# Kernel optimization log

Measured on AMD Instinct MI355X. Metric: run time of the kernel, lower is better.

The kernel has to match this reference:

```python
import jax, jax.numpy as jnp
import numpy as np

# Standard SMPL kinematic tree parents (kintree_table)
PARENTS = np.array([-1, 0, 0, 0, 1, 2, 3, 4, 5, 6, 7, 8, 9, 9, 9,
                    12, 13, 14, 16, 17, 18, 19, 20, 21])
NV, NJ, NB, NP = 6890, 24, 10, 207


def rodrigues(r):
    """Axis-angle [N,3] -> rotation matrices [N,3,3] (Rodrigues formula)."""
    theta = jnp.linalg.norm(r, axis=1, keepdims=True) + 1e-8  # [N,1]
    rh = r / theta                                            # [N,3]
    cos = jnp.cos(theta)[..., None]                           # [N,1,1]
    sin = jnp.sin(theta)[..., None]
    z = jnp.zeros_like(rh[:, 0])
    m = jnp.stack([z, -rh[:, 2], rh[:, 1],
                   rh[:, 2], z, -rh[:, 0],
                   -rh[:, 1], rh[:, 0], z], axis=1).reshape(-1, 3, 3)
    dot = rh[:, :, None] * rh[:, None, :]                     # outer product
    eye = jnp.eye(3, dtype=r.dtype)
    return cos * eye + (1.0 - cos) * dot + sin * m


def setup_inputs() -> dict:
    key = jax.random.key(0)
    ks = jax.random.split(key, 9)
    B = 512
    betas = jax.random.normal(ks[0], (B, NB), dtype=jnp.float32)
    thetas = jax.random.normal(ks[1], (B, NJ * 3), dtype=jnp.float32) * 0.3
    trans = jax.random.normal(ks[2], (B, 3), dtype=jnp.float32)
    scale = jnp.ones((1,), dtype=jnp.float32)
    v_template = jax.random.normal(ks[3], (NV, 3), dtype=jnp.float32)
    shapedirs = jax.random.normal(ks[4], (NV, 3, NB), dtype=jnp.float32) * 0.01
    posedirs = jax.random.normal(ks[5], (NV, 3, NP), dtype=jnp.float32) * 0.01
    Jr = jax.random.uniform(ks[6], (NJ, NV), dtype=jnp.float32)
    J_regressor = Jr / jnp.sum(Jr, axis=1, keepdims=True)
    w = jax.random.uniform(ks[7], (NV, NJ), dtype=jnp.float32)
    weights = w / jnp.sum(w, axis=1, keepdims=True)
    return {"betas": betas, "thetas": thetas, "trans": trans, "scale": scale,
            "v_template": v_template, "shapedirs": shapedirs,
            "posedirs": posedirs, "J_regressor": J_regressor,
            "weights": weights}


def reference(betas, thetas, trans, scale, v_template, shapedirs, posedirs,
              J_regressor, weights):
    B = betas.shape[0]
    dt = betas.dtype
    # Shape blend shapes: v_shaped [B, 6890, 3]
    v_shaped = jnp.einsum('bs,vcs->bvc', betas, shapedirs) + v_template
    # Rest-pose joints J(beta): [B, 24, 3]
    J = jnp.einsum('jv,bvc->bjc', J_regressor, v_shaped)
    # Local rotations from axis-angle, root scaled by `scale`
    lRs = rodrigues(thetas.reshape(-1, 3)).reshape(B, NJ, 3, 3)
    lRs = lRs.at[:, 0].multiply(scale[0])
    # Local joint offsets: root keeps J[:,0], children use J[i] - J[parent[i]]
    parents = jnp.asarray(PARENTS)
    t = J - J[:, jnp.clip(parents, 0)]
    t = t.at[:, 0].set(J[:, 0])
    # Local 4x4 transforms [B, 24, 4, 4]
    top = jnp.concatenate([lRs, t[..., None]], axis=3)          # [B,24,3,4]
    bottom = jnp.broadcast_to(jnp.array([0., 0., 0., 1.], dtype=dt),
                              (B, NJ, 1, 4))
    A = jnp.concatenate([top, bottom], axis=2)
    # Kinematic chain accumulation (fixed 24-joint tree)
    results = [A[:, 0]]
    for i in range(1, NJ):
        results.append(results[PARENTS[i]] @ A[:, i])
    stacked = jnp.stack(results, axis=1)                         # [B,24,4,4]
    # Remove rest-pose joint locations from translation column
    Jh = jnp.concatenate([J, jnp.zeros((B, NJ, 1), dtype=dt)], axis=2)
    deformed = jnp.einsum('bjxy,bjy->bjx', stacked, Jh)          # [B,24,4]
    G = stacked.at[..., 3].add(-deformed)
    # Pose blend shapes from non-root rotations
    lrotmin = (lRs[:, 1:] - jnp.eye(3, dtype=dt)).reshape(B, -1)  # [B,207]
    v_posed = v_shaped + jnp.einsum('bp,vcp->bvc', lrotmin, posedirs)
    # Linear blend skinning
    T = jnp.einsum('bjxy,vj->bvxy', G, weights)                  # [B,6890,4,4]
    vh = jnp.concatenate([v_posed, jnp.ones((B, NV, 1), dtype=dt)], axis=2)
    v = jnp.einsum('bvxy,bvy->bvx', T, vh)[:, :, :3]
    result = v + trans[:, None, :]
    joints = jnp.einsum('jv,bvc->bjc', J_regressor, result)
    return result, joints
```

## Files before the change

kernel.cpp:

```cpp
#include <hip/hip_runtime.h>

#define NVERT 6890
#define NJNT  24
#define NBETA 10
#define NPOSE 207
#define NBATCH 512
#define KPAD 224
#define MROWS 20736
#define NVC (NVERT * 3)

#define NBA 18144
#define NBW 1728
#define NJR 576

typedef __attribute__((ext_vector_type(8))) short short8;
typedef __attribute__((ext_vector_type(4))) float floatx4;

__constant__ int c_par[NJNT]   = {-1,0,0,0,1,2,3,4,5,6,7,8,9,9,9,12,13,14,16,17,18,19,20,21};
__constant__ int c_depth[NJNT] = { 0,1,1,1,2,2,2,3,3,3,4,4,4,4,4,5,5,5,6,6,7,7,8,8};

static __device__ __forceinline__ unsigned short f2bf(float x) {
  union { float f; unsigned u; } v; v.f = x;
  unsigned r = (v.u + 0x7FFFu + ((v.u >> 16) & 1u)) >> 16;
  return (unsigned short)r;
}
static __device__ __forceinline__ float bf2f(unsigned short h) {
  union { unsigned u; float f; } v; v.u = (unsigned)h << 16;
  return v.f;
}

typedef __attribute__((address_space(1))) const void as1_void;
typedef __attribute__((address_space(3))) void as3_void;
static __device__ __forceinline__ void gl_lds16(const void* g, void* l) {
  __builtin_amdgcn_global_load_lds((as1_void*)g, (as3_void*)l, 16, 0, 0);
}

__global__ __launch_bounds__(256) void k_prep(
    const float* __restrict__ pdir, const float* __restrict__ sd,
    const float* __restrict__ vt, const float* __restrict__ wgt,
    const float* __restrict__ Jr,
    unsigned short* __restrict__ AT, unsigned short* __restrict__ W16,
    float* __restrict__ wsJP) {
  const int bx = blockIdx.x;
  const int tid = threadIdx.x;
  if (bx < NBA) {
    const int idx = bx * 256 + tid;
    const int kk = idx & 31;
    const int row = (idx >> 5) % MROWS;
    const int kt = idx / (MROWS * 32);
    const int k = kt * 32 + kk;
    float val = 0.f;
    if (row < NVC) {
      if (k < NPOSE)            val = pdir[(size_t)row * NPOSE + k];
      else if (k < NPOSE + 10)  val = sd[(size_t)row * 10 + (k - NPOSE)];
      else if (k == NPOSE + 10) val = vt[row];
    }
    AT[idx] = f2bf(val);
  } else if (bx < NBA + NBW) {
    const int idx = (bx - NBA) * 256 + tid;
    const int v = idx >> 6, c = idx & 63, j = c & 31;
    const float w = (v < NVERT && j < 24) ? wgt[(size_t)v * 24 + j] : 0.f;
    const unsigned short hi = f2bf(w);
    W16[idx] = (c >> 5) ? f2bf(w - bf2f(hi)) : hi;
  } else {
    const int jb = bx - (NBA + NBW);
    const int jc = jb % 72, j = jc / 3, c = jc % 3;
    const int chunk = jb / 72;
    const int v0 = chunk * 864;
    const int vend = min(NVERT, v0 + 864);
    float acc[11];
    #pragma unroll
    for (int k = 0; k < 11; ++k) acc[k] = 0.f;
    for (int v = v0 + tid; v < vend; v += 256) {
      const float w = Jr[j * NVERT + v];
      acc[0] += w * vt[v * 3 + c];
      const float* s = sd + (size_t)v * 30 + c * 10;
      #pragma unroll
      for (int k = 0; k < 10; ++k) acc[1 + k] += w * s[k];
    }
    #pragma unroll
    for (int off = 32; off > 0; off >>= 1) {
      #pragma unroll
      for (int k = 0; k < 11; ++k) acc[k] += __shfl_down(acc[k], off, 64);
    }
    __shared__ float red[4][11];
    const int lane = tid & 63, wv = tid >> 6;
    if (lane == 0) {
      #pragma unroll
      for (int k = 0; k < 11; ++k) red[wv][k] = acc[k];
    }
    __syncthreads();
    if (tid == 0) {
      #pragma unroll
      for (int k = 0; k < 11; ++k)
        wsJP[(size_t)(chunk * 72 + jc) * 11 + k] =
            red[0][k] + red[1][k] + red[2][k] + red[3][k];
    }
  }
}

__global__ __launch_bounds__(256, 2) void k_chain3(
    const float* __restrict__ betas, const float* __restrict__ thetas,
    const float* __restrict__ scale, const float* __restrict__ trans,
    const float* __restrict__ wsJP,
    unsigned short* __restrict__ BT, unsigned short* __restrict__ G16) {
  __shared__ __align__(16) float sJ[792];
  __shared__ __align__(16) float sJJ[4][72];
  __shared__ __align__(16) float sM[4][288];
  __shared__ __align__(16) unsigned short sG[4][1024];
  __shared__ __align__(16) unsigned short sB[4][KPAD];

  const int tid = threadIdx.x;
  const int wv = tid >> 6, lane = tid & 63;
  const int b = blockIdx.x * 4 + wv;

  if (tid < 72) {
    #pragma unroll
    for (int k = 0; k < 11; ++k) {
      float s = 0.f;
      #pragma unroll
      for (int c8 = 0; c8 < 8; ++c8) s += wsJP[(size_t)(c8 * 72 + tid) * 11 + k];
      if (k == 0) sJ[tid] = s;
      else        sJ[72 + tid * 10 + (k - 1)] = s;
    }
  }
  #pragma unroll
  for (int r = 0; r < 4; ++r) {
    sG[wv][lane * 16 + r * 4 + 0] = 0; sG[wv][lane * 16 + r * 4 + 1] = 0;
    sG[wv][lane * 16 + r * 4 + 2] = 0; sG[wv][lane * 16 + r * 4 + 3] = 0;
  }
  __syncthreads();

  float R[9], t[3], M[12], Jx = 0.f, Jy = 0.f, Jz = 0.f;
  const int i = lane;
  if (i < NJNT) {
    #pragma unroll
    for (int c = 0; c < 3; ++c) {
      float a = sJ[i * 3 + c];
      const float* d = sJ + 72 + (i * 3 + c) * 10;
      #pragma unroll
      for (int s = 0; s < NBETA; ++s) a += d[s] * betas[b * NBETA + s];
      if (c == 0) Jx = a; else if (c == 1) Jy = a; else Jz = a;
    }
    sJJ[wv][i * 3 + 0] = Jx; sJJ[wv][i * 3 + 1] = Jy; sJJ[wv][i * 3 + 2] = Jz;
    const float rx = thetas[b * 72 + i * 3 + 0];
    const float ry = thetas[b * 72 + i * 3 + 1];
    const float rz = thetas[b * 72 + i * 3 + 2];
    const float th = sqrtf(rx * rx + ry * ry + rz * rz) + 1e-8f;
    const float inv = 1.f / th;
    const float x = rx * inv, y = ry * inv, z = rz * inv;
    const float cs = cosf(th), sn = sinf(th), omc = 1.f - cs;
    R[0] = cs + omc * x * x;     R[1] = omc * x * y - sn * z; R[2] = omc * x * z + sn * y;
    R[3] = omc * x * y + sn * z; R[4] = cs + omc * y * y;     R[5] = omc * y * z - sn * x;
    R[6] = omc * x * z - sn * y; R[7] = omc * y * z + sn * x; R[8] = cs + omc * z * z;
    if (i == 0) {
      const float sc = scale[0];
      #pragma unroll
      for (int k = 0; k < 9; ++k) R[k] *= sc;
    } else {
      #pragma unroll
      for (int k = 0; k < 9; ++k)
        sB[wv][(i - 1) * 9 + k] = f2bf(R[k] - ((k == 0 || k == 4 || k == 8) ? 1.f : 0.f));
    }
  }
  if (i == 0) {
    #pragma unroll
    for (int s = 0; s < NBETA; ++s) sB[wv][NPOSE + s] = f2bf(betas[b * NBETA + s]);
    sB[wv][NPOSE + 10] = 0x3F80;
    #pragma unroll
    for (int k = NPOSE + 11; k < KPAD; ++k) sB[wv][k] = 0;
  }
  __syncthreads();

  if (i < NJNT) {
    if (i == 0) { t[0] = Jx; t[1] = Jy; t[2] = Jz; }
    else {
      const int p = c_par[i];
      t[0] = Jx - sJJ[wv][p * 3 + 0];
      t[1] = Jy - sJJ[wv][p * 3 + 1];
      t[2] = Jz - sJJ[wv][p * 3 + 2];
    }
    if (i == 0) {
      #pragma unroll
      for (int r = 0; r < 3; ++r) {
        M[r*4+0] = R[r*3+0]; M[r*4+1] = R[r*3+1]; M[r*4+2] = R[r*3+2]; M[r*4+3] = t[r];
      }
      #pragma unroll
      for (int k = 0; k < 12; ++k) sM[wv][k] = M[k];
    }
  }
  __syncthreads();

  for (int lvl = 1; lvl <= 8; ++lvl) {
    if (i < NJNT && c_depth[i] == lvl) {
      const float* Mp = sM[wv] + c_par[i] * 12;
      #pragma unroll
      for (int r = 0; r < 3; ++r) {
        const float p0 = Mp[r*4+0], p1 = Mp[r*4+1], p2 = Mp[r*4+2], p3 = Mp[r*4+3];
        M[r*4+0] = p0*R[0] + p1*R[3] + p2*R[6];
        M[r*4+1] = p0*R[1] + p1*R[4] + p2*R[7];
        M[r*4+2] = p0*R[2] + p1*R[5] + p2*R[8];
        M[r*4+3] = p0*t[0] + p1*t[1] + p2*t[2] + p3;
      }
      #pragma unroll
      for (int k = 0; k < 12; ++k) sM[wv][i * 12 + k] = M[k];
    }
    __syncthreads();
  }

  if (i < NJNT) {
    #pragma unroll
    for (int r = 0; r < 3; ++r) {
      M[r*4+3] = M[r*4+3] - (M[r*4+0]*Jx + M[r*4+1]*Jy + M[r*4+2]*Jz)
               + trans[b * 3 + r];
    }
    #pragma unroll
    for (int e = 0; e < 12; ++e) {
      const float g = M[e];
      const unsigned short hi = f2bf(g);
      sG[wv][e * 32 + i]       = hi;
      sG[wv][512 + e * 32 + i] = f2bf(g - bf2f(hi));
    }
  }
  __syncthreads();

  *(uint4*)(G16 + (size_t)b * 1024 + lane * 16)     = *(uint4*)&sG[wv][lane * 16];
  *(uint4*)(G16 + (size_t)b * 1024 + lane * 16 + 8) = *(uint4*)&sG[wv][lane * 16 + 8];
  if (lane < 28)
    *(uint4*)(BT + ((size_t)(lane >> 2) * NBATCH + b) * 32 + (lane & 3) * 8) =
        *(uint4*)&sB[wv][lane * 8];
}

__global__ __launch_bounds__(256, 3) void k_skin4(
    const unsigned short* __restrict__ AT, const unsigned short* __restrict__ BT,
    const unsigned short* __restrict__ W16, const unsigned short* __restrict__ G16,
    float* __restrict__ out) {
  __shared__ __align__(16) char smem[33536];
  float* sV           = (float*)smem;
  unsigned short* sG2 = (unsigned short*)(smem + 13056);

  const int tid = threadIdx.x;
  const int wv = tid >> 6, lane = tid & 63;
  const int q = lane >> 4, n = lane & 15;

  const int fb = blockIdx.x;
  const int vb = (fb & 7) * 108 + (fb >> 3);
  const int b0 = (vb & 7) * 64;
  const int by = vb >> 3;
  const int vc0 = by * 192;

  floatx4 acc[3][4];
  #pragma unroll
  for (int mt = 0; mt < 3; ++mt)
    #pragma unroll
    for (int nt = 0; nt < 4; ++nt) acc[mt][nt] = (floatx4)(0.f);

  const int stoff = (lane >> 2) * 32 + (((lane & 3) ^ ((lane >> 3) & 3)) * 8);
  const int rslot = ((lane >> 4) ^ ((lane >> 1) & 3)) * 8;

  const unsigned short* gA0 = AT + ((size_t)vc0 + 48 * wv) * 32 + stoff;
  const unsigned short* gB0 = BT + ((size_t)b0 + 16 * wv) * 32 + stoff;

  {
    unsigned short* la = (unsigned short*)smem + 48 * wv * 32;
    unsigned short* lb = (unsigned short*)(smem + 12288) + 16 * wv * 32;
    gl_lds16(gA0,        la);
    gl_lds16(gA0 + 512,  la + 512);
    gl_lds16(gA0 + 1024, la + 1024);
    gl_lds16(gB0,        lb);
  }
  __syncthreads();

  int cur = 0;
  for (int kt = 0; kt < 7; ++kt) {
    if (kt < 6) {
      const int nb = (cur ^ 1) << 14;
      unsigned short* la = (unsigned short*)(smem + nb) + 48 * wv * 32;
      unsigned short* lb = (unsigned short*)(smem + nb + 12288) + 16 * wv * 32;
      const unsigned short* ga = gA0 + (size_t)(kt + 1) * MROWS * 32;
      const unsigned short* gb = gB0 + (size_t)(kt + 1) * NBATCH * 32;
      gl_lds16(ga,        la);
      gl_lds16(ga + 512,  la + 512);
      gl_lds16(ga + 1024, la + 1024);
      gl_lds16(gb,        lb);
    }
    const unsigned short* sAc = (const unsigned short*)(smem + (cur << 14));
    const unsigned short* sBc = sAc + 6144;
    short8 af[3], bfr[4];
    #pragma unroll
    for (int mt = 0; mt < 3; ++mt)
      af[mt] = *(const short8*)(sAc + (48 * wv + 16 * mt + n) * 32 + rslot);
    #pragma unroll
    for (int nt = 0; nt < 4; ++nt)
      bfr[nt] = *(const short8*)(sBc + (16 * nt + n) * 32 + rslot);
    #pragma unroll
    for (int mt = 0; mt < 3; ++mt)
      #pragma unroll
      for (int nt = 0; nt < 4; ++nt)
        acc[mt][nt] = __builtin_amdgcn_mfma_f32_16x16x32_bf16(
            af[mt], bfr[nt], acc[mt][nt], 0, 0, 0);
    __syncthreads();
    cur ^= 1;
  }

  short8 wh[4], wl[4];
  #pragma unroll
  for (int vt = 0; vt < 4; ++vt) {
    const unsigned short* wr = W16 + (size_t)(by * 64 + vt * 16 + n) * 64;
    wh[vt] = *(const short8*)(wr + q * 8);
    wl[vt] = *(const short8*)(wr + 32 + q * 8);
  }

  for (int nt = 0; nt < 4; ++nt) {
    for (int s = 0; s < 2; ++s) {
      __syncthreads();
      if (s == 0) {
        #pragma unroll
        for (int mt = 0; mt < 3; ++mt)
          #pragma unroll
          for (int r = 0; r < 4; ++r)
            sV[(48 * wv + 16 * mt + 4 * q + r) * 17 + n] = acc[mt][nt][r];
      }
      const int bg0 = b0 + nt * 16 + s * 8;
      for (int i = tid; i < 1024; i += 256) {
        const int row = i >> 2, c4 = i & 3;
        const int t = row >> 5, rem = row & 31;
        *(uint4*)(sG2 + row * 40 + c4 * 8) =
            *(const uint4*)(G16 + (size_t)(bg0 + t) * 1024 + rem * 32 + c4 * 8);
      }
      __syncthreads();
      #pragma unroll
      for (int bb = 0; bb < 2; ++bb) {
        const int t = wv * 2 + bb;
        const int col = s * 8 + t;
        const int bg = b0 + nt * 16 + col;
        const short8 gh = *(const short8*)(sG2 + (t * 32 + n) * 40 + q * 8);
        const short8 gl = *(const short8*)(sG2 + (t * 32 + 16 + n) * 40 + q * 8);
        #pragma unroll
        for (int vt = 0; vt < 4; ++vt) {
          floatx4 a2 = (floatx4)(0.f);
          a2 = __builtin_amdgcn_mfma_f32_16x16x32_bf16(gh, wl[vt], a2, 0, 0, 0);
          a2 = __builtin_amdgcn_mfma_f32_16x16x32_bf16(gl, wh[vt], a2, 0, 0, 0);
          a2 = __builtin_amdgcn_mfma_f32_16x16x32_bf16(gh, wh[vt], a2, 0, 0, 0);
          const float X = sV[(48 * vt + 3 * n + 0) * 17 + col];
          const float Y = sV[(48 * vt + 3 * n + 1) * 17 + col];
          const float Z = sV[(48 * vt + 3 * n + 2) * 17 + col];
          const float o = a2[0] * X + a2[1] * Y + a2[2] * Z + a2[3];
          const int vc = vc0 + 48 * vt + 3 * n + q;
          if (q < 3 && vc < NVC)
            out[(size_t)bg * NVC + vc] = o;
        }
      }
    }
  }
}

__global__ __launch_bounds__(256) void k_jnt1(
    const float* __restrict__ Jr, const float* __restrict__ res,
    float* __restrict__ wsJ2) {
  const int b0 = blockIdx.x * 2;
  const int chunk = blockIdx.y;
  const int v0 = chunk * 864;
  const int vend = min(NVERT, v0 + 864);
  const int lane = threadIdx.x & 63, wv = threadIdx.x >> 6;
  float acc[36];
  #pragma unroll
  for (int k = 0; k < 36; ++k) acc[k] = 0.f;
  const float* rA = res + (size_t)b0 * NVC;
  const float* rB = res + (size_t)(b0 + 1) * NVC;
  for (int v = v0 + lane; v < vend; v += 64) {
    const float a0 = rA[v * 3 + 0], a1 = rA[v * 3 + 1], a2 = rA[v * 3 + 2];
    const float e0 = rB[v * 3 + 0], e1 = rB[v * 3 + 1], e2 = rB[v * 3 + 2];
    #pragma unroll
    for (int k = 0; k < 6; ++k) {
      const int j = wv + 4 * k;
      const float w = Jr[j * NVERT + v];
      acc[k*6+0] += w * a0; acc[k*6+1] += w * a1; acc[k*6+2] += w * a2;
      acc[k*6+3] += w * e0; acc[k*6+4] += w * e1; acc[k*6+5] += w * e2;
    }
  }
  #pragma unroll
  for (int off = 32; off > 0; off >>= 1) {
    #pragma unroll
    for (int k = 0; k < 36; ++k) acc[k] += __shfl_down(acc[k], off, 64);
  }
  if (lane == 0) {
    #pragma unroll
    for (int k = 0; k < 6; ++k) {
      const int j = wv + 4 * k;
      float* d0 = wsJ2 + ((size_t)b0 * 8 + chunk) * 72 + j * 3;
      d0[0] = acc[k*6+0]; d0[1] = acc[k*6+1]; d0[2] = acc[k*6+2];
      float* d1 = wsJ2 + ((size_t)(b0 + 1) * 8 + chunk) * 72 + j * 3;
      d1[0] = acc[k*6+3]; d1[1] = acc[k*6+4]; d1[2] = acc[k*6+5];
    }
  }
}

__global__ __launch_bounds__(256) void k_jnt2(
    const float* __restrict__ wsJ2, float* __restrict__ joints) {
  const int idx = blockIdx.x * 256 + threadIdx.x;
  const int b = idx / 72, jc = idx - b * 72;
  float s = 0.f;
  #pragma unroll
  for (int c8 = 0; c8 < 8; ++c8)
    s += wsJ2[((size_t)b * 8 + c8) * 72 + jc];
  joints[idx] = s;
}

extern "C" void kernel_launch(void* const* d_in, const int* in_sizes, int n_in,
                              void* d_out, int out_size, void* d_ws, size_t ws_size,
                              hipStream_t stream) {
  const float* betas  = (const float*)d_in[0];
  const float* thetas = (const float*)d_in[1];
  const float* trans  = (const float*)d_in[2];
  const float* scale  = (const float*)d_in[3];
  const float* vtpl   = (const float*)d_in[4];
  const float* sd     = (const float*)d_in[5];
  const float* pdir   = (const float*)d_in[6];
  const float* Jr     = (const float*)d_in[7];
  const float* wgt    = (const float*)d_in[8];
  float* out = (float*)d_out;

  float* ws   = (float*)d_ws;
  float* wsJP = ws;
  unsigned short* AT  = (unsigned short*)(ws + 6336);
  unsigned short* BT  = AT + (size_t)MROWS * KPAD;
  unsigned short* W16 = BT + (size_t)NBATCH * KPAD;
  unsigned short* G16 = W16 + (size_t)6912 * 64;
  float* wsJ2 = (float*)AT;

  k_prep<<<NBA + NBW + NJR, 256, 0, stream>>>(pdir, sd, vtpl, wgt, Jr, AT, W16, wsJP);
  k_chain3<<<NBATCH / 4, 256, 0, stream>>>(betas, thetas, scale, trans, wsJP, BT, G16);
  k_skin4<<<864, 256, 0, stream>>>(AT, BT, W16, G16, out);
  k_jnt1<<<dim3(NBATCH / 2, 8), 256, 0, stream>>>(Jr, out, wsJ2);
  k_jnt2<<<(NBATCH * 72) / 256, 256, 0, stream>>>(wsJ2, out + (size_t)NBATCH * NVC);
}
```

Baseline: 173.9 us.

## Halve skinning batch tile and replace joint reduction kernel with atomics

```diff
diff --git a/kernel.cpp b/kernel.cpp
--- a/kernel.cpp
+++ b/kernel.cpp
@@ -103,7 +103,8 @@
     const float* __restrict__ betas, const float* __restrict__ thetas,
     const float* __restrict__ scale, const float* __restrict__ trans,
     const float* __restrict__ wsJP,
-    unsigned short* __restrict__ BT, unsigned short* __restrict__ G16) {
+    unsigned short* __restrict__ BT, unsigned short* __restrict__ G16,
+    float* __restrict__ jzero) {
   __shared__ __align__(16) float sJ[792];
   __shared__ __align__(16) float sJJ[4][72];
   __shared__ __align__(16) float sM[4][288];
@@ -113,6 +114,9 @@
   const int tid = threadIdx.x;
   const int wv = tid >> 6, lane = tid & 63;
   const int b = blockIdx.x * 4 + wv;
+
+  for (int z = blockIdx.x * 256 + tid; z < NBATCH * 72; z += 32768)
+    jzero[z] = 0.f;
 
   if (tid < 72) {
     #pragma unroll
@@ -231,7 +235,7 @@
         *(uint4*)&sB[wv][lane * 8];
 }
 
-__global__ __launch_bounds__(256, 3) void k_skin4(
+__global__ __launch_bounds__(256, 4) void k_skin4(
     const unsigned short* __restrict__ AT, const unsigned short* __restrict__ BT,
     const unsigned short* __restrict__ W16, const unsigned short* __restrict__ G16,
     float* __restrict__ out) {
@@ -244,16 +248,16 @@
   const int q = lane >> 4, n = lane & 15;
 
   const int fb = blockIdx.x;
-  const int vb = (fb & 7) * 108 + (fb >> 3);
-  const int b0 = (vb & 7) * 64;
-  const int by = vb >> 3;
+  const int vb = (fb & 7) * 216 + (fb >> 3);
+  const int b0 = (vb & 15) * 32;
+  const int by = vb >> 4;
   const int vc0 = by * 192;
 
-  floatx4 acc[3][4];
+  floatx4 acc[3][2];
   #pragma unroll
   for (int mt = 0; mt < 3; ++mt)
     #pragma unroll
-    for (int nt = 0; nt < 4; ++nt) acc[mt][nt] = (floatx4)(0.f);
+    for (int nt = 0; nt < 2; ++nt) acc[mt][nt] = (floatx4)(0.f);
 
   const int stoff = (lane >> 2) * 32 + (((lane & 3) ^ ((lane >> 3) & 3)) * 8);
   const int rslot = ((lane >> 4) ^ ((lane >> 1) & 3)) * 8;
@@ -263,40 +267,43 @@
 
   {
     unsigned short* la = (unsigned short*)smem + 48 * wv * 32;
-    unsigned short* lb = (unsigned short*)(smem + 12288) + 16 * wv * 32;
     gl_lds16(gA0,        la);
     gl_lds16(gA0 + 512,  la + 512);
     gl_lds16(gA0 + 1024, la + 1024);
-    gl_lds16(gB0,        lb);
+    if (wv < 2) {
+      unsigned short* lb = (unsigned short*)(smem + 12288) + 16 * wv * 32;
+      gl_lds16(gB0, lb);
+    }
   }
   __syncthreads();
 
   int cur = 0;
   for (int kt = 0; kt < 7; ++kt) {
     if (kt < 6) {
-      const int nb = (cur ^ 1) << 14;
+      const int nb = (cur ^ 1) * 14336;
       unsigned short* la = (unsigned short*)(smem + nb) + 48 * wv * 32;
-      unsigned short* lb = (unsigned short*)(smem + nb + 12288) + 16 * wv * 32;
       const unsigned short* ga = gA0 + (size_t)(kt + 1) * MROWS * 32;
-      const unsigned short* gb = gB0 + (size_t)(kt + 1) * NBATCH * 32;
       gl_lds16(ga,        la);
       gl_lds16(ga + 512,  la + 512);
       gl_lds16(ga + 1024, la + 1024);
-      gl_lds16(gb,        lb);
-    }
-    const unsigned short* sAc = (const unsigned short*)(smem + (cur << 14));
+      if (wv < 2) {
+        unsigned short* lb = (unsigned short*)(smem + nb + 12288) + 16 * wv * 32;
+        gl_lds16(gB0 + (size_t)(kt + 1) * NBATCH * 32, lb);
+      }
+    }
+    const unsigned short* sAc = (const unsigned short*)(smem + cur * 14336);
     const unsigned short* sBc = sAc + 6144;
-    short8 af[3], bfr[4];
+    short8 af[3], bfr[2];
     #pragma unroll
     for (int mt = 0; mt < 3; ++mt)
       af[mt] = *(const short8*)(sAc + (48 * wv + 16 * mt + n) * 32 + rslot);
     #pragma unroll
-    for (int nt = 0; nt < 4; ++nt)
+    for (int nt = 0; nt < 2; ++nt)
       bfr[nt] = *(const short8*)(sBc + (16 * nt + n) * 32 + rslot);
     #pragma unroll
     for (int mt = 0; mt < 3; ++mt)
       #pragma unroll
-      for (int nt = 0; nt < 4; ++nt)
+      for (int nt = 0; nt < 2; ++nt)
         acc[mt][nt] = __builtin_amdgcn_mfma_f32_16x16x32_bf16(
             af[mt], bfr[nt], acc[mt][nt], 0, 0, 0);
     __syncthreads();
@@ -311,7 +318,7 @@
     wl[vt] = *(const short8*)(wr + 32 + q * 8);
   }
 
-  for (int nt = 0; nt < 4; ++nt) {
+  for (int nt = 0; nt < 2; ++nt) {
     for (int s = 0; s < 2; ++s) {
       __syncthreads();
       if (s == 0) {
@@ -357,7 +364,7 @@
 
 __global__ __launch_bounds__(256) void k_jnt1(
     const float* __restrict__ Jr, const float* __restrict__ res,
-    float* __restrict__ wsJ2) {
+    float* __restrict__ joints) {
   const int b0 = blockIdx.x * 2;
   const int chunk = blockIdx.y;
   const int v0 = chunk * 864;
@@ -388,23 +395,14 @@
     #pragma unroll
     for (int k = 0; k < 6; ++k) {
       const int j = wv + 4 * k;
-      float* d0 = wsJ2 + ((size_t)b0 * 8 + chunk) * 72 + j * 3;
-      d0[0] = acc[k*6+0]; d0[1] = acc[k*6+1]; d0[2] = acc[k*6+2];
-      float* d1 = wsJ2 + ((size_t)(b0 + 1) * 8 + chunk) * 72 + j * 3;
-      d1[0] = acc[k*6+3]; d1[1] = acc[k*6+4]; d1[2] = acc[k*6+5];
-    }
-  }
-}
-
-__global__ __launch_bounds__(256) void k_jnt2(
-    const float* __restrict__ wsJ2, float* __restrict__ joints) {
-  const int idx = blockIdx.x * 256 + threadIdx.x;
-  const int b = idx / 72, jc = idx - b * 72;
-  float s = 0.f;
-  #pragma unroll
-  for (int c8 = 0; c8 < 8; ++c8)
-    s += wsJ2[((size_t)b * 8 + c8) * 72 + jc];
-  joints[idx] = s;
+      atomicAdd(&joints[(size_t)b0 * 72 + j * 3 + 0], acc[k*6+0]);
+      atomicAdd(&joints[(size_t)b0 * 72 + j * 3 + 1], acc[k*6+1]);
+      atomicAdd(&joints[(size_t)b0 * 72 + j * 3 + 2], acc[k*6+2]);
+      atomicAdd(&joints[(size_t)(b0 + 1) * 72 + j * 3 + 0], acc[k*6+3]);
+      atomicAdd(&joints[(size_t)(b0 + 1) * 72 + j * 3 + 1], acc[k*6+4]);
+      atomicAdd(&joints[(size_t)(b0 + 1) * 72 + j * 3 + 2], acc[k*6+5]);
+    }
+  }
 }
 
 extern "C" void kernel_launch(void* const* d_in, const int* in_sizes, int n_in,
@@ -420,6 +418,7 @@
   const float* Jr     = (const float*)d_in[7];
   const float* wgt    = (const float*)d_in[8];
   float* out = (float*)d_out;
+  float* joints = out + (size_t)NBATCH * NVC;
 
   float* ws   = (float*)d_ws;
   float* wsJP = ws;
@@ -427,11 +426,9 @@
   unsigned short* BT  = AT + (size_t)MROWS * KPAD;
   unsigned short* W16 = BT + (size_t)NBATCH * KPAD;
   unsigned short* G16 = W16 + (size_t)6912 * 64;
-  float* wsJ2 = (float*)AT;
 
   k_prep<<<NBA + NBW + NJR, 256, 0, stream>>>(pdir, sd, vtpl, wgt, Jr, AT, W16, wsJP);
-  k_chain3<<<NBATCH / 4, 256, 0, stream>>>(betas, thetas, scale, trans, wsJP, BT, G16);
-  k_skin4<<<864, 256, 0, stream>>>(AT, BT, W16, G16, out);
-  k_jnt1<<<dim3(NBATCH / 2, 8), 256, 0, stream>>>(Jr, out, wsJ2);
-  k_jnt2<<<(NBATCH * 72) / 256, 256, 0, stream>>>(wsJ2, out + (size_t)NBATCH * NVC);
-}
+  k_chain3<<<NBATCH / 4, 256, 0, stream>>>(betas, thetas, scale, trans, wsJP, BT, G16, joints);
+  k_skin4<<<1728, 256, 0, stream>>>(AT, BT, W16, G16, out);
+  k_jnt1<<<dim3(NBATCH / 2, 8), 256, 0, stream>>>(Jr, out, joints);
+}
```

Measured after the change: 180.6 us. +3.9%, slower.
